# Optimization experiments

Measured on AMD Instinct MI355X. Metric: run time of the kernel, lower is better.

Reference implementation:

```python
import jax, jax.numpy as jnp
import numpy as np

B, S, D = 4, 4096, 256


def setup_inputs() -> dict:
    key = jax.random.key(0)
    ks = jax.random.split(key, 8)
    inv = 1.0 / np.sqrt(D)
    return {
        "input_tensor": jax.random.normal(ks[0], (B, S, D), dtype=jnp.float32),
        "attention_mask": jax.random.randint(ks[1], (B, S, S), 0, 2) == 1,
        "Wq": jax.random.uniform(ks[2], (D, D), jnp.float32, -inv, inv),
        "bq": jax.random.uniform(ks[3], (D,), jnp.float32, -inv, inv),
        "Wk": jax.random.uniform(ks[4], (D, D), jnp.float32, -inv, inv),
        "bk": jax.random.uniform(ks[5], (D,), jnp.float32, -inv, inv),
        "Wv": jax.random.uniform(ks[6], (D, D), jnp.float32, -inv, inv),
        "bv": jax.random.uniform(ks[7], (D,), jnp.float32, -inv, inv),
    }


def reference(input_tensor, attention_mask, Wq, bq, Wk, bk, Wv, bv):
    # Linear projections: y = x @ W.T + b  (nn.Linear convention, W is [out,in])
    query = jnp.einsum("bsd,ed->bse", input_tensor, Wq) + bq
    key = jnp.einsum("bsd,ed->bse", input_tensor, Wk) + bk
    value = jnp.einsum("bsd,ed->bse", input_tensor, Wv) + bv
    # Faithful quirk: original scales by sqrt(query.size(1)) == sqrt(seq_len)
    scale = jnp.asarray(query.shape[1], query.dtype) ** 0.5
    scores = jnp.einsum("bqd,bkd->bqk", query, key) / scale  # [B,S,S]
    scores = jnp.where(attention_mask, jnp.asarray(-1e9, scores.dtype), scores)
    attn = jax.nn.softmax(scores, axis=-1)
    # dropout with p=0.0 is identity (eval-mode reference)
    context = jnp.einsum("bqk,bkd->bqd", attn, value)
    return context
```

## Files before the change

kernel.cpp:

```cpp
#include <hip/hip_runtime.h>
#include <hip/hip_bf16.h>
#include <stdint.h>

#define BB 4
#define SS 4096
#define DD 256

typedef __attribute__((ext_vector_type(4))) float f32x4;
typedef __attribute__((ext_vector_type(8))) short s16x8;

__device__ __forceinline__ ushort f2bf(float f) {
  __hip_bfloat16 h = __float2bfloat16(f);
  return __builtin_bit_cast(ushort, h);
}

__global__ void convert_kernel(const float* __restrict__ X,
                               const float* __restrict__ Wq,
                               const float* __restrict__ Wk,
                               const float* __restrict__ Wv,
                               const float* __restrict__ bq,
                               const float* __restrict__ bk,
                               const float* __restrict__ bv,
                               ushort* __restrict__ Xb,
                               ushort* __restrict__ Wb,
                               float* __restrict__ bias) {
  int tid = blockIdx.x * blockDim.x + threadIdx.x;
  int stride = gridDim.x * blockDim.x;
  const int NX4 = (BB * SS * DD) / 4;
  for (int i = tid; i < NX4; i += stride) {
    float4 v = ((const float4*)X)[i];
    ushort4 o = { f2bf(v.x), f2bf(v.y), f2bf(v.z), f2bf(v.w) };
    ((ushort4*)Xb)[i] = o;
  }
  const int NW4 = (DD * DD) / 4;
  for (int i = tid; i < NW4; i += stride) {
    float4 a = ((const float4*)Wq)[i];
    float4 b = ((const float4*)Wk)[i];
    float4 c = ((const float4*)Wv)[i];
    ushort4 oa = { f2bf(a.x), f2bf(a.y), f2bf(a.z), f2bf(a.w) };
    ushort4 ob = { f2bf(b.x), f2bf(b.y), f2bf(b.z), f2bf(b.w) };
    ushort4 oc = { f2bf(c.x), f2bf(c.y), f2bf(c.z), f2bf(c.w) };
    ((ushort4*)Wb)[i]           = oa;
    ((ushort4*)Wb)[NW4 + i]     = ob;
    ((ushort4*)Wb)[2 * NW4 + i] = oc;
  }
  if (tid < DD) {
    bias[tid]          = bq[tid];
    bias[DD + tid]     = bk[tid];
    bias[2 * DD + tid] = bv[tid];
  }
}

#define LROW 40

__global__ __launch_bounds__(256) void proj_gemm(const ushort* __restrict__ Xb,
                                                 const ushort* __restrict__ Wb,
                                                 const float* __restrict__ bias,
                                                 ushort* __restrict__ Qb,
                                                 ushort* __restrict__ Kb,
                                                 ushort* __restrict__ Vt) {
  __shared__ ushort Al[128 * LROW];
  __shared__ ushort Bl[128 * LROW];
  const int m0 = blockIdx.x * 128;
  const int n0 = blockIdx.y * 128;
  const int t = threadIdx.x;
  const int lane = t & 63;
  const int w = t >> 6;
  const int wr = w & 1, wc = w >> 1;
  const int col = lane & 15;
  const int quad = lane >> 4;

  f32x4 acc[4][4];
#pragma unroll
  for (int i = 0; i < 4; i++)
#pragma unroll
    for (int j = 0; j < 4; j++) acc[i][j] = f32x4{0.f, 0.f, 0.f, 0.f};

  const int ci0 = t, ci1 = 256 + t;
  const int r0 = ci0 >> 2, c0 = ci0 & 3;
  const int r1 = ci1 >> 2, c1 = ci1 & 3;

  s16x8 pa0 = *(const s16x8*)(Xb + (m0 + r0) * DD + c0 * 8);
  s16x8 pa1 = *(const s16x8*)(Xb + (m0 + r1) * DD + c1 * 8);
  s16x8 pb0 = *(const s16x8*)(Wb + (n0 + r0) * DD + c0 * 8);
  s16x8 pb1 = *(const s16x8*)(Wb + (n0 + r1) * DD + c1 * 8);

  for (int kk = 0; kk < DD; kk += 32) {
    __syncthreads();
    *(s16x8*)&Al[r0 * LROW + c0 * 8] = pa0;
    *(s16x8*)&Al[r1 * LROW + c1 * 8] = pa1;
    *(s16x8*)&Bl[r0 * LROW + c0 * 8] = pb0;
    *(s16x8*)&Bl[r1 * LROW + c1 * 8] = pb1;
    __syncthreads();
    const int kn = kk + 32;
    if (kn < DD) {
      pa0 = *(const s16x8*)(Xb + (m0 + r0) * DD + kn + c0 * 8);
      pa1 = *(const s16x8*)(Xb + (m0 + r1) * DD + kn + c1 * 8);
      pb0 = *(const s16x8*)(Wb + (n0 + r0) * DD + kn + c0 * 8);
      pb1 = *(const s16x8*)(Wb + (n0 + r1) * DD + kn + c1 * 8);
    }
    s16x8 af[4], bfr[4];
#pragma unroll
    for (int mi = 0; mi < 4; mi++)
      af[mi] = *(const s16x8*)&Al[(wr * 64 + mi * 16 + col) * LROW + quad * 8];
#pragma unroll
    for (int ni = 0; ni < 4; ni++)
      bfr[ni] = *(const s16x8*)&Bl[(wc * 64 + ni * 16 + col) * LROW + quad * 8];
#pragma unroll
    for (int mi = 0; mi < 4; mi++)
#pragma unroll
      for (int ni = 0; ni < 4; ni++)
        acc[mi][ni] = __builtin_amdgcn_mfma_f32_16x16x32_bf16(af[mi], bfr[ni], acc[mi][ni], 0, 0, 0);
  }

  const int region = n0 >> 8;
#pragma unroll
  for (int mi = 0; mi < 4; mi++) {
    const int gm = m0 + wr * 64 + mi * 16 + quad * 4;
#pragma unroll
    for (int ni = 0; ni < 4; ni++) {
      const int gn = n0 + wc * 64 + ni * 16 + col;
      const float bb = bias[gn];
      f32x4 v = acc[mi][ni];
      if (region == 0) {
#pragma unroll
        for (int rg = 0; rg < 4; rg++)
          Qb[(gm + rg) * DD + gn] = f2bf((v[rg] + bb) * 0.015625f);
      } else if (region == 1) {
        const int d = gn - 256;
#pragma unroll
        for (int rg = 0; rg < 4; rg++)
          Kb[(gm + rg) * DD + d] = f2bf(v[rg] + bb);
      } else {
        const int d = gn - 512;
        const int b = gm >> 12;
        const int s = gm & (SS - 1);
        ushort4 o = { f2bf(v[0] + bb), f2bf(v[1] + bb), f2bf(v[2] + bb), f2bf(v[3] + bb) };
        *(ushort4*)&Vt[((size_t)(b << 8) + d) * SS + s] = o;
      }
    }
  }
}

#define NKT 32
#define KROW 264
#define VROW 32
#define PROW 32

#define KVREG_U 8448
#define PL_U (16 * PROW)
#define POFF (2 * KVREG_U)
#define SM_U (POFF + 8 * PL_U)

#define XSTRIDE 72

__global__ __launch_bounds__(512) void attn_kernel(const ushort* __restrict__ Qb,
                                                   const ushort* __restrict__ Kb,
                                                   const ushort* __restrict__ Vt,
                                                   const int* __restrict__ mask,
                                                   float* __restrict__ out,
                                                   float* __restrict__ O1,
                                                   float* __restrict__ Ml) {
  __shared__ __align__(16) ushort sm[SM_U];

  const int qt = blockIdx.x;
  const int b = blockIdx.y;
  const int z = blockIdx.z;
  const int t = threadIdx.x;
  const int g = t >> 8;
  const int tg = t & 255;
  const int lane = t & 63;
  const int w = tg >> 6;
  const int w8 = t >> 6;
  const int col = lane & 15;
  const int quad = lane >> 4;

  ushort* Kl = sm + g * KVREG_U;
  ushort* Vl = sm + g * KVREG_U;
  ushort* Pw = sm + POFF + w8 * PL_U;

  const int q0 = qt * 64;
  const int qrow = q0 + w * 16;

  s16x8 qf[8];
  {
    const ushort* qp = Qb + ((size_t)b * SS + qrow + col) * DD + quad * 8;
#pragma unroll
    for (int dc = 0; dc < 8; dc++) qf[dc] = *(const s16x8*)(qp + dc * 32);
  }

  int kr[4], kc[4], vd[4], vc[4];
#pragma unroll
  for (int i = 0; i < 4; i++) {
    const int ci = i * 256 + tg;
    kr[i] = ci >> 5; kc[i] = ci & 31;
    vd[i] = ci >> 2; vc[i] = ci & 3;
  }

  const ushort* Kg = Kb + (size_t)b * SS * DD;
  const ushort* Vg = Vt + (size_t)b * DD * SS;
  const int* Mg = mask + ((size_t)b * SS + qrow + quad * 4) * SS;

  f32x4 Oc[16];
#pragma unroll
  for (int i = 0; i < 16; i++) Oc[i] = f32x4{0.f, 0.f, 0.f, 0.f};
  float m_i[4] = {-INFINITY, -INFINITY, -INFINITY, -INFINITY};
  float l_i[4] = {0.f, 0.f, 0.f, 0.f};

  const int NT2 = 1024 / NKT;
  const int kb0 = z * 2048 + g * 1024;

  s16x8 pk[4], pv[4];
  int pm[2][4];
#pragma unroll
  for (int i = 0; i < 4; i++) {
    pk[i] = *(const s16x8*)(Kg + (size_t)(kb0 + kr[i]) * DD + kc[i] * 8);
    pv[i] = *(const s16x8*)(Vg + (size_t)vd[i] * SS + kb0 + vc[i] * 8);
  }
#pragma unroll
  for (int jt = 0; jt < 2; jt++)
#pragma unroll
    for (int rg = 0; rg < 4; rg++) pm[jt][rg] = Mg[rg * SS + kb0 + jt * 16 + col];

  for (int tt = 0; tt < NT2; tt++) {
    __syncthreads();
#pragma unroll
    for (int i = 0; i < 4; i++)
      *(s16x8*)&Kl[kr[i] * KROW + kc[i] * 8] = pk[i];
    __syncthreads();
    int mcur[2][4];
#pragma unroll
    for (int jt = 0; jt < 2; jt++)
#pragma unroll
      for (int rg = 0; rg < 4; rg++) mcur[jt][rg] = pm[jt][rg];
    const int k0n = kb0 + (tt + 1) * NKT;
    if (tt + 1 < NT2) {
#pragma unroll
      for (int i = 0; i < 4; i++)
        pk[i] = *(const s16x8*)(Kg + ((size_t)k0n + kr[i]) * DD + kc[i] * 8);
#pragma unroll
      for (int jt = 0; jt < 2; jt++)
#pragma unroll
        for (int rg = 0; rg < 4; rg++) pm[jt][rg] = Mg[rg * SS + k0n + jt * 16 + col];
    }

    f32x4 st[2];
    __builtin_amdgcn_s_setprio(1);
#pragma unroll
    for (int jt = 0; jt < 2; jt++) {
      f32x4 s = f32x4{0.f, 0.f, 0.f, 0.f};
#pragma unroll
      for (int dc = 0; dc < 8; dc++) {
        s16x8 kb = *(const s16x8*)&Kl[(jt * 16 + col) * KROW + dc * 32 + quad * 8];
        s = __builtin_amdgcn_mfma_f32_16x16x32_bf16(qf[dc], kb, s, 0, 0, 0);
      }
      st[jt] = s;
    }
    __builtin_amdgcn_s_setprio(0);
#pragma unroll
    for (int jt = 0; jt < 2; jt++)
#pragma unroll
      for (int rg = 0; rg < 4; rg++)
        if (mcur[jt][rg]) st[jt][rg] = -1e9f;

    float al[4];
#pragma unroll
    for (int rg = 0; rg < 4; rg++) {
      float v = fmaxf(st[0][rg], st[1][rg]);
      v = fmaxf(v, __shfl_xor(v, 1));
      v = fmaxf(v, __shfl_xor(v, 2));
      v = fmaxf(v, __shfl_xor(v, 4));
      v = fmaxf(v, __shfl_xor(v, 8));
      const float mn = fmaxf(m_i[rg], v);
      al[rg] = __expf(m_i[rg] - mn);
      m_i[rg] = mn;
    }
#pragma unroll
    for (int rg = 0; rg < 4; rg++) {
      const float p0 = __expf(st[0][rg] - m_i[rg]);
      const float p1 = __expf(st[1][rg] - m_i[rg]);
      st[0][rg] = p0; st[1][rg] = p1;
      float s2 = p0 + p1;
      s2 += __shfl_xor(s2, 1);
      s2 += __shfl_xor(s2, 2);
      s2 += __shfl_xor(s2, 4);
      s2 += __shfl_xor(s2, 8);
      l_i[rg] = l_i[rg] * al[rg] + s2;
    }

#pragma unroll
    for (int jt = 0; jt < 2; jt++)
#pragma unroll
      for (int rg = 0; rg < 4; rg++)
        Pw[(quad * 4 + rg) * PROW + jt * 16 + col] = f2bf(st[jt][rg]);
    s16x8 pa = *(const s16x8*)&Pw[col * PROW + quad * 8];

#pragma unroll
    for (int dt = 0; dt < 16; dt++)
#pragma unroll
      for (int rg = 0; rg < 4; rg++) Oc[dt][rg] *= al[rg];

    __syncthreads();
#pragma unroll
    for (int i = 0; i < 4; i++)
      *(s16x8*)&Vl[vd[i] * VROW + vc[i] * 8] = pv[i];
    if (tt + 1 < NT2) {
#pragma unroll
      for (int i = 0; i < 4; i++)
        pv[i] = *(const s16x8*)(Vg + (size_t)vd[i] * SS + k0n + vc[i] * 8);
    }
    __syncthreads();

    __builtin_amdgcn_s_setprio(1);
#pragma unroll
    for (int dt = 0; dt < 16; dt++) {
      s16x8 vb = *(const s16x8*)&Vl[(dt * 16 + col) * VROW + quad * 8];
      Oc[dt] = __builtin_amdgcn_mfma_f32_16x16x32_bf16(pa, vb, Oc[dt], 0, 0, 0);
    }
    __builtin_amdgcn_s_setprio(0);
  }

  float* ex = (float*)sm;
#pragma unroll
  for (int rr = 0; rr < 2; rr++) {
    __syncthreads();
    if (g == 1 && (w >> 1) == rr) {
      float* slot = ex + (size_t)((w & 1) * 64 + lane) * XSTRIDE;
#pragma unroll
      for (int rg = 0; rg < 4; rg++) { slot[rg] = m_i[rg]; slot[4 + rg] = l_i[rg]; }
#pragma unroll
      for (int dt = 0; dt < 16; dt++) *(f32x4*)&slot[8 + dt * 4] = Oc[dt];
    }
    __syncthreads();
    if (g == 0 && (w >> 1) == rr) {
      const float* slot = ex + (size_t)((w & 1) * 64 + lane) * XSTRIDE;
      float a0[4], a1[4];
#pragma unroll
      for (int rg = 0; rg < 4; rg++) {
        const float m1 = slot[rg];
        const float l1 = slot[4 + rg];
        const float mm = fmaxf(m_i[rg], m1);
        a0[rg] = __expf(m_i[rg] - mm);
        a1[rg] = __expf(m1 - mm);
        m_i[rg] = mm;
        l_i[rg] = l_i[rg] * a0[rg] + l1 * a1[rg];
      }
#pragma unroll
      for (int dt = 0; dt < 16; dt++) {
        const f32x4 o1 = *(const f32x4*)&slot[8 + dt * 4];
#pragma unroll
        for (int rg = 0; rg < 4; rg++)
          Oc[dt][rg] = Oc[dt][rg] * a0[rg] + o1[rg] * a1[rg];
      }
    }
  }
  if (g == 0) {
    float* op = (z ? O1 : out) + ((size_t)b * SS + qrow + quad * 4) * DD;
#pragma unroll
    for (int dt = 0; dt < 16; dt++) {
#pragma unroll
      for (int rg = 0; rg < 4; rg++)
        op[rg * DD + dt * 16 + col] = Oc[dt][rg];
    }
    if (col == 0) {
      float2* pml = (float2*)Ml + (size_t)z * BB * SS + (size_t)b * SS + qrow + quad * 4;
#pragma unroll
      for (int rg = 0; rg < 4; rg++) pml[rg] = make_float2(m_i[rg], l_i[rg]);
    }
  }
}

__global__ __launch_bounds__(256) void merge_kernel(const float* __restrict__ Ml,
                                                    const float* __restrict__ O1,
                                                    float* __restrict__ out) {
  const int row = blockIdx.x * 4 + (threadIdx.x >> 6);
  const int lane = threadIdx.x & 63;
  const float2 ml0 = ((const float2*)Ml)[row];
  const float2 ml1 = ((const float2*)Ml)[BB * SS + row];
  const float mm = fmaxf(ml0.x, ml1.x);
  const float a0 = __expf(ml0.x - mm);
  const float a1 = __expf(ml1.x - mm);
  const float inv = 1.0f / (ml0.y * a0 + ml1.y * a1);
  f32x4* po = (f32x4*)out + (size_t)row * 64 + lane;
  const f32x4 o0 = *po;
  const f32x4 o1 = ((const f32x4*)O1)[(size_t)row * 64 + lane];
  f32x4 r;
#pragma unroll
  for (int j = 0; j < 4; j++) r[j] = (o0[j] * a0 + o1[j] * a1) * inv;
  *po = r;
}

extern "C" void kernel_launch(void* const* d_in, const int* in_sizes, int n_in,
                              void* d_out, int out_size, void* d_ws, size_t ws_size,
                              hipStream_t stream) {
  const float* X  = (const float*)d_in[0];
  const int* mask = (const int*)d_in[1];
  const float* Wq = (const float*)d_in[2];
  const float* bq = (const float*)d_in[3];
  const float* Wk = (const float*)d_in[4];
  const float* bk = (const float*)d_in[5];
  const float* Wv = (const float*)d_in[6];
  const float* bv = (const float*)d_in[7];
  float* out = (float*)d_out;

  ushort* base = (ushort*)d_ws;
  ushort* Xb = base;
  ushort* Wb = Xb + (size_t)BB * SS * DD;
  ushort* Qb = Wb + (size_t)3 * DD * DD;
  ushort* Kb = Qb + (size_t)BB * SS * DD;
  ushort* Vt = Kb + (size_t)BB * SS * DD;
  float* bias = (float*)(Vt + (size_t)BB * SS * DD);
  float* O1 = bias + 768;
  float* Ml = O1 + (size_t)BB * SS * DD;

  convert_kernel<<<1024, 256, 0, stream>>>(X, Wq, Wk, Wv, bq, bk, bv, Xb, Wb, bias);
  proj_gemm<<<dim3(128, 6), 256, 0, stream>>>(Xb, Wb, bias, Qb, Kb, Vt);
  attn_kernel<<<dim3(64, 4, 2), 512, 0, stream>>>(Qb, Kb, Vt, mask, out, O1, Ml);
  merge_kernel<<<(BB * SS) / 4, 256, 0, stream>>>(Ml, O1, out);
}
```

Before: 513.7 us.

## Pack attention mask into bitmasks and skip no-op output rescaling

```diff
diff --git a/kernel.cpp b/kernel.cpp
--- a/kernel.cpp
+++ b/kernel.cpp
@@ -51,6 +51,20 @@
   }
 }
 
+__global__ void maskpack_kernel(const int* __restrict__ mask,
+                                unsigned long long* __restrict__ Pm) {
+  const int tid = blockIdx.x * blockDim.x + threadIdx.x;
+  const int wid = tid >> 6;
+  const int lane = tid & 63;
+  const int nw = (gridDim.x * blockDim.x) >> 6;
+  const int NP = (BB * SS * SS) / 64;
+  for (int i = wid; i < NP; i += nw) {
+    const int v = mask[(size_t)i * 64 + lane];
+    const unsigned long long bal = __ballot(v != 0);
+    if (lane == 0) Pm[i] = bal;
+  }
+}
+
 #define LROW 40
 
 __global__ __launch_bounds__(256) void proj_gemm(const ushort* __restrict__ Xb,
@@ -146,6 +160,7 @@
 #define KROW 264
 #define VROW 32
 #define PROW 32
+#define MROW (SS / 32)
 
 #define KVREG_U 8448
 #define PL_U (16 * PROW)
@@ -157,7 +172,7 @@
 __global__ __launch_bounds__(512) void attn_kernel(const ushort* __restrict__ Qb,
                                                    const ushort* __restrict__ Kb,
                                                    const ushort* __restrict__ Vt,
-                                                   const int* __restrict__ mask,
+                                                   const uint* __restrict__ Pm,
                                                    float* __restrict__ out,
                                                    float* __restrict__ O1,
                                                    float* __restrict__ Ml) {
@@ -199,7 +214,7 @@
 
   const ushort* Kg = Kb + (size_t)b * SS * DD;
   const ushort* Vg = Vt + (size_t)b * DD * SS;
-  const int* Mg = mask + ((size_t)b * SS + qrow + quad * 4) * SS;
+  const uint* MgP = Pm + ((size_t)b * SS + qrow + quad * 4) * MROW;
 
   f32x4 Oc[16];
 #pragma unroll
@@ -211,16 +226,14 @@
   const int kb0 = z * 2048 + g * 1024;
 
   s16x8 pk[4], pv[4];
-  int pm[2][4];
+  uint pmw[4];
 #pragma unroll
   for (int i = 0; i < 4; i++) {
     pk[i] = *(const s16x8*)(Kg + (size_t)(kb0 + kr[i]) * DD + kc[i] * 8);
     pv[i] = *(const s16x8*)(Vg + (size_t)vd[i] * SS + kb0 + vc[i] * 8);
   }
 #pragma unroll
-  for (int jt = 0; jt < 2; jt++)
-#pragma unroll
-    for (int rg = 0; rg < 4; rg++) pm[jt][rg] = Mg[rg * SS + kb0 + jt * 16 + col];
+  for (int rg = 0; rg < 4; rg++) pmw[rg] = MgP[rg * MROW + (kb0 >> 5)];
 
   for (int tt = 0; tt < NT2; tt++) {
     __syncthreads();
@@ -228,20 +241,16 @@
     for (int i = 0; i < 4; i++)
       *(s16x8*)&Kl[kr[i] * KROW + kc[i] * 8] = pk[i];
     __syncthreads();
-    int mcur[2][4];
-#pragma unroll
-    for (int jt = 0; jt < 2; jt++)
-#pragma unroll
-      for (int rg = 0; rg < 4; rg++) mcur[jt][rg] = pm[jt][rg];
+    uint mcur[4];
+#pragma unroll
+    for (int rg = 0; rg < 4; rg++) mcur[rg] = pmw[rg];
     const int k0n = kb0 + (tt + 1) * NKT;
     if (tt + 1 < NT2) {
 #pragma unroll
       for (int i = 0; i < 4; i++)
         pk[i] = *(const s16x8*)(Kg + ((size_t)k0n + kr[i]) * DD + kc[i] * 8);
 #pragma unroll
-      for (int jt = 0; jt < 2; jt++)
-#pragma unroll
-        for (int rg = 0; rg < 4; rg++) pm[jt][rg] = Mg[rg * SS + k0n + jt * 16 + col];
+      for (int rg = 0; rg < 4; rg++) pmw[rg] = MgP[rg * MROW + (k0n >> 5)];
     }
 
     f32x4 st[2];
@@ -261,7 +270,7 @@
     for (int jt = 0; jt < 2; jt++)
 #pragma unroll
       for (int rg = 0; rg < 4; rg++)
-        if (mcur[jt][rg]) st[jt][rg] = -1e9f;
+        if ((mcur[rg] >> (jt * 16 + col)) & 1u) st[jt][rg] = -1e9f;
 
     float al[4];
 #pragma unroll
@@ -295,10 +304,15 @@
         Pw[(quad * 4 + rg) * PROW + jt * 16 + col] = f2bf(st[jt][rg]);
     s16x8 pa = *(const s16x8*)&Pw[col * PROW + quad * 8];
 
-#pragma unroll
-    for (int dt = 0; dt < 16; dt++)
-#pragma unroll
-      for (int rg = 0; rg < 4; rg++) Oc[dt][rg] *= al[rg];
+    {
+      const bool need = (al[0] < 1.f) | (al[1] < 1.f) | (al[2] < 1.f) | (al[3] < 1.f);
+      if (__any(need)) {
+#pragma unroll
+        for (int dt = 0; dt < 16; dt++)
+#pragma unroll
+          for (int rg = 0; rg < 4; rg++) Oc[dt][rg] *= al[rg];
+      }
+    }
 
     __syncthreads();
 #pragma unroll
@@ -412,9 +426,12 @@
   float* bias = (float*)(Vt + (size_t)BB * SS * DD);
   float* O1 = bias + 768;
   float* Ml = O1 + (size_t)BB * SS * DD;
+  unsigned long long* Pm = (unsigned long long*)Xb;
 
   convert_kernel<<<1024, 256, 0, stream>>>(X, Wq, Wk, Wv, bq, bk, bv, Xb, Wb, bias);
   proj_gemm<<<dim3(128, 6), 256, 0, stream>>>(Xb, Wb, bias, Qb, Kb, Vt);
-  attn_kernel<<<dim3(64, 4, 2), 512, 0, stream>>>(Qb, Kb, Vt, mask, out, O1, Ml);
+  maskpack_kernel<<<1024, 256, 0, stream>>>(mask, Pm);
+  attn_kernel<<<dim3(64, 4, 2), 512, 0, stream>>>(Qb, Kb, Vt, (const uint*)Pm,
+                                                  out, O1, Ml);
   merge_kernel<<<(BB * SS) / 4, 256, 0, stream>>>(Ml, O1, out);
 }
```

Result: slower. 679.7 us (+32.3%).
